# Kernel tuning notes

Measured on AMD Instinct MI355X. Metric: run time of the kernel, lower is better.

Reference implementation:

```python
import jax, jax.numpy as jnp
import numpy as np
from jax import lax

K = 3            # RFAConv kernel size
CIN = 66         # RFAConv in_channel = c2/2 + 2
UP = 64          # up channel count = c2/2
BN_EPS = 1e-5


def conv2d(x, w, stride=1, padding=0, groups=1, bias=None):
    out = lax.conv_general_dilated(
        x, w, (stride, stride), [(padding, padding), (padding, padding)],
        dimension_numbers=("NCHW", "OIHW", "NCHW"), feature_group_count=groups)
    if bias is not None:
        out = out + bias[None, :, None, None]
    return out


def avgpool3(x):
    # AvgPool2d(kernel=3, pad=1, stride=1), count_include_pad=True -> /9 everywhere
    s = lax.reduce_window(x, 0.0, lax.add, (1, 1, 3, 3), (1, 1, 1, 1),
                          [(0, 0), (0, 0), (1, 1), (1, 1)])
    return s / 9.0


def setup_inputs() -> dict:
    key = jax.random.key(0)
    ks = jax.random.split(key, 8)
    c1, c2 = 64, 128
    inp = {
        "x": jax.random.normal(ks[0], (8, c1, 256, 256), jnp.float32),
        "w_squeeze": jax.random.normal(ks[1], (c2, 4 * c1, 1, 1), jnp.float32) * 0.05,
        "w_gw": jax.random.normal(ks[2], (CIN * K * K, 1, 1, 1), jnp.float32) * 0.3,
        "w_gf": jax.random.normal(ks[3], (CIN * K * K, 1, K, K), jnp.float32) * 0.3,
        "bn_gamma": jnp.ones((CIN * K * K,), jnp.float32),
        "bn_beta": jnp.zeros((CIN * K * K,), jnp.float32),
        "bn_mean": jnp.zeros((CIN * K * K,), jnp.float32),
        "bn_var": jnp.ones((CIN * K * K,), jnp.float32),
        "w_conv": jax.random.normal(ks[4], (UP, CIN, K, K), jnp.float32) * 0.05,
        "b_conv": jnp.zeros((UP,), jnp.float32),
    }
    return inp


def reference(x, w_squeeze, w_gw, w_gf, bn_gamma, bn_beta, bn_mean, bn_var,
              w_conv, b_conv):
    # space_to_depth: [B,C,H,W] -> [B,4C,H/2,W/2]
    x = jnp.concatenate([x[..., ::2, ::2], x[..., 1::2, ::2],
                         x[..., ::2, 1::2], x[..., 1::2, 1::2]], axis=1)
    # squeeze0: 1x1 conv 4*c1 -> c2
    x = conv2d(x, w_squeeze)
    up, low = x[:, :UP], x[:, UP:]

    # AddCoords (with_r=False): append normalized xx (width) and yy (height)
    b, _, h, w = up.shape
    xx = (jnp.arange(w, dtype=up.dtype) / (w - 1) * 2.0 - 1.0)
    yy = (jnp.arange(h, dtype=up.dtype) / (h - 1) * 2.0 - 1.0)
    xx = jnp.broadcast_to(xx[None, None, None, :], (b, 1, h, w))
    yy = jnp.broadcast_to(yy[None, None, :, None], (b, 1, h, w))
    up = jnp.concatenate([up, xx, yy], axis=1)   # [b, 66, h, w]

    # RFAConv
    weight = conv2d(avgpool3(up), w_gw, groups=CIN)          # [b, 594, h, w]
    weight = jax.nn.softmax(weight.reshape(b, CIN, K * K, h, w), axis=2)

    feat = conv2d(up, w_gf, stride=1, padding=1, groups=CIN)  # [b, 594, h, w]
    scale = bn_gamma / jnp.sqrt(bn_var + BN_EPS)
    shift = bn_beta - bn_mean * scale
    feat = jax.nn.relu(feat * scale[None, :, None, None] + shift[None, :, None, None])
    feat = feat.reshape(b, CIN, K * K, h, w)

    wd = feat * weight
    # rearrange 'b c (n1 n2) h w -> b c (h n1) (w n2)'
    wd = wd.reshape(b, CIN, K, K, h, w).transpose(0, 1, 4, 2, 5, 3)
    wd = wd.reshape(b, CIN, h * K, w * K)
    up = conv2d(wd, w_conv, stride=K, bias=b_conv)            # [b, 64, h, w]

    y = jnp.concatenate([up, low], axis=1)                    # [b, 128, h, w]
    # channel shuffle: gather even channels then odd channels
    bb, n, hh, ww = y.shape
    y = y.reshape(bb, n // 2, 2, hh, ww)
    return jnp.concatenate([y[:, :, 0], y[:, :, 1]], axis=1)
```

## Files before the change

### kernel.cpp

```cpp
#include <hip/hip_runtime.h>
#include <math.h>

typedef __attribute__((ext_vector_type(8))) short short8;
typedef __attribute__((ext_vector_type(4))) float f32x4;

#define B 8
#define H 128
#define W 128
#define UPC 64
#define CIN 66
#define BN_EPS 1e-5f

#define BSQ_U16  ((size_t)16777216)
#define BSQ_CNT  32768
#define BF_U16   (BSQ_U16 + BSQ_CNT)
#define BF_CNT   38912
#define SC_F     ((size_t)8424448)
#define SH_F     (SC_F + 594)

static __device__ __forceinline__ unsigned short f2bf(float f) {
    unsigned u = __float_as_uint(f);
    u += 0x7fffu + ((u >> 16) & 1u);
    return (unsigned short)(u >> 16);
}
static __device__ __forceinline__ unsigned pack2(float lo, float hi) {
    return __builtin_amdgcn_perm(__float_as_uint(hi) + 0x8000u,
                                 __float_as_uint(lo) + 0x8000u, 0x07060302u);
}

__global__ void prep_kernel(const float* __restrict__ w_squeeze,
                            const float* __restrict__ gamma,
                            const float* __restrict__ beta,
                            const float* __restrict__ mean,
                            const float* __restrict__ var,
                            const float* __restrict__ w_conv,
                            float* __restrict__ ws)
{
    unsigned short* wsu = (unsigned short*)ws;
    int tid = blockIdx.x * blockDim.x + threadIdx.x;
    int nth = gridDim.x * blockDim.x;

    for (int idx = tid; idx < BSQ_CNT; idx += nth) {
        int j = idx & 7, lane = (idx >> 3) & 63, r = idx >> 9;
        int nt = r & 7, kc = r >> 3;
        int k = kc * 32 + ((lane >> 4) << 3) + j;
        int n = nt * 16 + (lane & 15);
        wsu[BSQ_U16 + idx] = f2bf(w_squeeze[n * 256 + k]);
    }
    for (int idx = tid; idx < BF_CNT; idx += nth) {
        int j = idx & 7, lane = (idx >> 3) & 63, r = idx >> 9;
        int nt = r & 3, ks = r >> 2;
        int k = ks * 32 + ((lane >> 4) << 3) + j;
        int n = nt * 16 + (lane & 15);
        float v = (k < 594) ? w_conv[n * 594 + k] : 0.f;
        wsu[BF_U16 + idx] = f2bf(v);
    }
    for (int i = tid; i < CIN * 9; i += nth) {
        float sc = gamma[i] / sqrtf(var[i] + BN_EPS);
        ws[SC_F + i] = sc;
        ws[SH_F + i] = beta[i] - mean[i] * sc;
    }
}

__global__ __launch_bounds__(256, 4) void squeeze_mfma(
    const float* __restrict__ x,
    float* __restrict__ wsp,
    float* __restrict__ out)
{
    __shared__ uint4 As[32 * 64];

    const int m0 = blockIdx.x * 64;
    const int w0 = m0 & 127;
    const int h  = (m0 >> 7) & 127;
    const int b  = m0 >> 14;
    const int tid  = threadIdx.x;
    const int lane = tid & 63;
    const int wv   = tid >> 6;
    const int oct = tid >> 5;
    const int pp  = tid & 31;

    float4 v[2][8];
#pragma unroll
    for (int gy = 0; gy < 2; ++gy)
#pragma unroll
        for (int i = 0; i < 8; ++i)
            v[gy][i] = *(const float4*)(x +
                (size_t)(b * 64 + oct * 8 + i) * 65536 +
                (2 * h + gy) * 256 + 2 * w0 + 4 * pp);

#pragma unroll
    for (int gy = 0; gy < 2; ++gy)
#pragma unroll
        for (int gx = 0; gx < 2; ++gx)
#pragma unroll
            for (int p = 0; p < 2; ++p) {
                const int comp = p * 2 + gx;
                uint4 u;
                u.x = pack2(((const float*)&v[gy][0])[comp], ((const float*)&v[gy][1])[comp]);
                u.y = pack2(((const float*)&v[gy][2])[comp], ((const float*)&v[gy][3])[comp]);
                u.z = pack2(((const float*)&v[gy][4])[comp], ((const float*)&v[gy][5])[comp]);
                u.w = pack2(((const float*)&v[gy][6])[comp], ((const float*)&v[gy][7])[comp]);
                As[((gy + 2 * gx) * 8 + oct) * 64 + 2 * pp + p] = u;
            }

    const unsigned short* bsq = (const unsigned short*)wsp + BSQ_U16;
    short8 breg[2][8];
#pragma unroll
    for (int ks = 0; ks < 8; ++ks)
#pragma unroll
        for (int j = 0; j < 2; ++j)
            breg[j][ks] = *(const short8*)(bsq +
                (size_t)((ks * 8 + (2 * wv + j)) * 64 + lane) * 8);

    __syncthreads();

    const int q = lane >> 4, m = lane & 15;
    f32x4 acc[4][2];
#pragma unroll
    for (int mt = 0; mt < 4; ++mt)
#pragma unroll
        for (int j = 0; j < 2; ++j) acc[mt][j] = (f32x4){0.f, 0.f, 0.f, 0.f};

#pragma unroll
    for (int ks = 0; ks < 8; ++ks)
#pragma unroll
        for (int mt = 0; mt < 4; ++mt) {
            short8 a = *(const short8*)&As[(ks * 4 + q) * 64 + mt * 16 + m];
            acc[mt][0] = __builtin_amdgcn_mfma_f32_16x16x32_bf16(a, breg[0][ks], acc[mt][0], 0, 0, 0);
            acc[mt][1] = __builtin_amdgcn_mfma_f32_16x16x32_bf16(a, breg[1][ks], acc[mt][1], 0, 0, 0);
        }

    if (wv < 2) {
        unsigned short* upw = (unsigned short*)wsp;
#pragma unroll
        for (int j = 0; j < 2; ++j) {
            const int oc = (2 * wv + j) * 16 + m;
#pragma unroll
            for (int mt = 0; mt < 4; ++mt) {
                uint2 st;
                st.x = pack2(acc[mt][j][0], acc[mt][j][1]);
                st.y = pack2(acc[mt][j][2], acc[mt][j][3]);
                *(uint2*)(upw + (size_t)(b * 64 + oc) * 16384 + h * 128
                          + (w0 + mt * 16 + q * 4)) = st;
            }
        }
    } else {
#pragma unroll
        for (int j = 0; j < 2; ++j) {
            const int oc = (2 * wv + j) * 16 + m;
            const int lc = oc - 64;
            const int ch = (lc & 1) ? (96 + ((lc - 1) >> 1)) : (32 + (lc >> 1));
#pragma unroll
            for (int mt = 0; mt < 4; ++mt) {
                float4 st = {acc[mt][j][0], acc[mt][j][1], acc[mt][j][2], acc[mt][j][3]};
                *(float4*)(out + ((size_t)(b * 128 + ch) * 128 + h) * 128
                           + (w0 + mt * 16 + q * 4)) = st;
            }
        }
    }
}

__device__ __forceinline__ void fs_from_n(
    int cu, const float n[9],
    const float* __restrict__ w_gw, const float* __restrict__ w_gf,
    const float* __restrict__ scp, const float* __restrict__ shp,
    float fs[9])
{
    const float p = (n[0] + n[1] + n[2] + n[3] + n[4] + n[5] + n[6] + n[7] + n[8]) * (1.f / 9.f);
    const float* gw = w_gw + cu * 9;
    const float* gf = w_gf + cu * 81;
    const float* sc = scp + cu * 9;
    const float* sh = shp + cu * 9;
    float e[9], se = 0.f;
#pragma unroll
    for (int j = 0; j < 9; ++j) { e[j] = __expf(p * gw[j]); se += e[j]; }
    const float sinv = 1.f / se;
#pragma unroll
    for (int j = 0; j < 9; ++j) {
        float cv = n[0] * gf[j * 9 + 0];
        cv = fmaf(n[1], gf[j * 9 + 1], cv); cv = fmaf(n[2], gf[j * 9 + 2], cv);
        cv = fmaf(n[3], gf[j * 9 + 3], cv); cv = fmaf(n[4], gf[j * 9 + 4], cv);
        cv = fmaf(n[5], gf[j * 9 + 5], cv); cv = fmaf(n[6], gf[j * 9 + 6], cv);
        cv = fmaf(n[7], gf[j * 9 + 7], cv); cv = fmaf(n[8], gf[j * 9 + 8], cv);
        float f = fmaf(cv, sc[j], sh[j]);
        fs[j] = fmaxf(f, 0.f) * (e[j] * sinv);
    }
}

__device__ __forceinline__ void pack_into(unsigned* pk, int ci, const float fs[9], float& carry)
{
    const int off = 9 * ci;
    if ((ci & 1) == 0) {
#pragma unroll
        for (int t = 0; t < 4; ++t) pk[off / 2 + t] = pack2(fs[2 * t], fs[2 * t + 1]);
        carry = fs[8];
    } else {
        pk[(off - 1) / 2] = pack2(carry, fs[0]);
#pragma unroll
        for (int t = 0; t < 4; ++t) pk[(off + 1) / 2 + t] = pack2(fs[1 + 2 * t], fs[2 + 2 * t]);
    }
}

template<bool BORDER>
__device__ __forceinline__ void chunk_fs(
    int cs, int wv, int lane, int h0, int w0,
    const unsigned short* __restrict__ upb,
    const float* __restrict__ w_gw, const float* __restrict__ w_gf,
    const float* __restrict__ scp, const float* __restrict__ shp,
    unsigned pk[36])
{
    const int px = lane & 7, py = lane >> 3;
    const int gy0 = h0 + py - 1;
    const int gxc = w0 + px;
    float carry = 0.f;

    if (!BORDER) {
        const int gx0 = (gxc - 1) & ~1;
        const unsigned sh = (gxc & 1) ? 0u : 16u;
        const size_t rowoff = (size_t)gy0 * 128 + gx0;
#pragma unroll
        for (int ci = 0; ci < 8; ++ci) {
            const int cu = __builtin_amdgcn_readfirstlane(cs + 8 * wv + ci);
            const unsigned short* cb = upb + (size_t)cu * 16384 + rowoff;
            float n[9];
#pragma unroll
            for (int dy = 0; dy < 3; ++dy) {
                const uint2 v = *(const uint2*)(cb + dy * 128);
                unsigned long long t = (((unsigned long long)v.y) << 32) | v.x;
                t >>= sh;
                n[dy * 3 + 0] = __uint_as_float((unsigned)t << 16);
                n[dy * 3 + 1] = __uint_as_float((unsigned)t & 0xffff0000u);
                n[dy * 3 + 2] = __uint_as_float((unsigned)(t >> 32) << 16);
            }
            float fs[9];
            fs_from_n(cu, n, w_gw, w_gf, scp, shp, fs);
            pack_into(pk, ci, fs, carry);
        }
    } else {
#pragma unroll
        for (int ci = 0; ci < 8; ++ci) {
            const int cu = __builtin_amdgcn_readfirstlane(cs + 8 * wv + ci);
            const unsigned short* cb = upb + (size_t)cu * 16384;
            float n[9];
#pragma unroll
            for (int dy = 0; dy < 3; ++dy)
#pragma unroll
                for (int dx = 0; dx < 3; ++dx) {
                    const int gy = gy0 + dy, gx = gxc - 1 + dx;
                    const bool ok = ((unsigned)gy < 128u) & ((unsigned)gx < 128u);
                    const int cy = min(max(gy, 0), 127), cx = min(max(gx, 0), 127);
                    const float f = __uint_as_float((unsigned)cb[cy * 128 + cx] << 16);
                    n[dy * 3 + dx] = ok ? f : 0.f;
                }
            float fs[9];
            fs_from_n(cu, n, w_gw, w_gf, scp, shp, fs);
            pack_into(pk, ci, fs, carry);
        }
    }
}

__device__ __forceinline__ void coord_n(int which, int h0, int w0, int lane, float n[9])
{
    const int px = lane & 7, py = lane >> 3;
#pragma unroll
    for (int dy = 0; dy < 3; ++dy)
#pragma unroll
        for (int dx = 0; dx < 3; ++dx) {
            const int gy = h0 + py - 1 + dy, gx = w0 + px - 1 + dx;
            const bool ok = ((unsigned)gy < 128u) & ((unsigned)gx < 128u);
            const float v = (which == 0) ? (gx * (2.f / 127.f) - 1.f)
                                         : (gy * (2.f / 127.f) - 1.f);
            n[dy * 3 + dx] = ok ? v : 0.f;
        }
}

template<int NSTEPS>
__device__ __forceinline__ void do_mfma(
    int base, const uint4* As, const unsigned short* __restrict__ bfw,
    int wv, int lane, f32x4 acc[2][2])
{
    const int q = lane >> 4, m = lane & 15;
    const int ntb = (wv >> 1) * 2;
    const int pt0 = (wv & 1) * 2;
#pragma unroll
    for (int ks = 0; ks < NSTEPS; ++ks) {
        short8 b0 = *(const short8*)(bfw + (size_t)(((base + ks) * 4 + ntb + 0) * 64 + lane) * 8);
        short8 b1 = *(const short8*)(bfw + (size_t)(((base + ks) * 4 + ntb + 1) * 64 + lane) * 8);
#pragma unroll
        for (int mt = 0; mt < 2; ++mt) {
            short8 a = *(const short8*)&As[(ks * 4 + q) * 64 + (pt0 + mt) * 16 + m];
            acc[mt][0] = __builtin_amdgcn_mfma_f32_16x16x32_bf16(a, b0, acc[mt][0], 0, 0, 0);
            acc[mt][1] = __builtin_amdgcn_mfma_f32_16x16x32_bf16(a, b1, acc[mt][1], 0, 0, 0);
        }
    }
}

__global__ __launch_bounds__(256, 4) void fused_mfma(
    const float* __restrict__ wsp,
    const float* __restrict__ w_gw,
    const float* __restrict__ w_gf,
    const float* __restrict__ b_conv,
    float* __restrict__ out)
{
    __shared__ uint4 As[40 * 64];

    const int bx = blockIdx.x;
    const int w0 = (bx & 15) * 8;
    const int h0 = ((bx >> 4) & 15) * 8;
    const int b  = bx >> 8;
    const int tid = threadIdx.x, lane = tid & 63, wv = tid >> 6;
    const bool interior = (h0 > 0) & (h0 < 120) & (w0 > 0) & (w0 < 120);

    const unsigned short* upb = (const unsigned short*)wsp + (size_t)b * UPC * 16384;
    const float* scp = wsp + SC_F;
    const float* shp = wsp + SH_F;
    const unsigned short* bfw = (const unsigned short*)wsp + BF_U16;

    f32x4 acc[2][2];
#pragma unroll
    for (int mt = 0; mt < 2; ++mt)
#pragma unroll
        for (int j = 0; j < 2; ++j) acc[mt][j] = (f32x4){0.f, 0.f, 0.f, 0.f};

    {
        unsigned pk[36];
        if (interior) chunk_fs<false>(0, wv, lane, h0, w0, upb, w_gw, w_gf, scp, shp, pk);
        else          chunk_fs<true >(0, wv, lane, h0, w0, upb, w_gw, w_gf, scp, shp, pk);
        __syncthreads();
#pragma unroll
        for (int kb = 0; kb < 9; ++kb)
            As[(9 * wv + kb) * 64 + lane] =
                (uint4){pk[4 * kb], pk[4 * kb + 1], pk[4 * kb + 2], pk[4 * kb + 3]};
        __syncthreads();
        do_mfma<9>(0, As, bfw, wv, lane, acc);
    }

    {
        unsigned pk[36];
        if (interior) chunk_fs<false>(32, wv, lane, h0, w0, upb, w_gw, w_gf, scp, shp, pk);
        else          chunk_fs<true >(32, wv, lane, h0, w0, upb, w_gw, w_gf, scp, shp, pk);

        float fsA[9], fsB[9];
        if (wv == 3) {
            float n2[9];
            coord_n(0, h0, w0, lane, n2);
            fs_from_n(64, n2, w_gw, w_gf, scp, shp, fsA);
            coord_n(1, h0, w0, lane, n2);
            fs_from_n(65, n2, w_gw, w_gf, scp, shp, fsB);
        }
        __syncthreads();
#pragma unroll
        for (int kb = 0; kb < 9; ++kb)
            As[(9 * wv + kb) * 64 + lane] =
                (uint4){pk[4 * kb], pk[4 * kb + 1], pk[4 * kb + 2], pk[4 * kb + 3]};
        if (wv == 3) {
            uint4 v;
            v.x = pack2(fsA[0], fsA[1]); v.y = pack2(fsA[2], fsA[3]);
            v.z = pack2(fsA[4], fsA[5]); v.w = pack2(fsA[6], fsA[7]);
            As[36 * 64 + lane] = v;
            v.x = pack2(fsA[8], fsB[0]); v.y = pack2(fsB[1], fsB[2]);
            v.z = pack2(fsB[3], fsB[4]); v.w = pack2(fsB[5], fsB[6]);
            As[37 * 64 + lane] = v;
            v.x = pack2(fsB[7], fsB[8]); v.y = 0u; v.z = 0u; v.w = 0u;
            As[38 * 64 + lane] = v;
            v.x = 0u; v.y = 0u; v.z = 0u; v.w = 0u;
            As[39 * 64 + lane] = v;
        }
        __syncthreads();
        do_mfma<10>(9, As, bfw, wv, lane, acc);
    }

    const int q = lane >> 4, m = lane & 15;
    const int ntb = (wv >> 1) * 2, pt0 = (wv & 1) * 2;
#pragma unroll
    for (int mt = 0; mt < 2; ++mt)
#pragma unroll
        for (int j = 0; j < 2; ++j) {
            const int oc = (ntb + j) * 16 + m;
            const float bias = b_conv[oc];
            const int ch = (oc & 1) ? (64 + (oc >> 1)) : (oc >> 1);
#pragma unroll
            for (int r = 0; r < 4; ++r) {
                const int pix = (pt0 + mt) * 16 + q * 4 + r;
                out[((size_t)((b * 128 + ch) * 128 + (h0 + (pix >> 3)))) * 128
                    + (w0 + (pix & 7))] = acc[mt][j][r] + bias;
            }
        }
}

extern "C" void kernel_launch(void* const* d_in, const int* in_sizes, int n_in,
                              void* d_out, int out_size, void* d_ws, size_t ws_size,
                              hipStream_t stream)
{
    const float* x         = (const float*)d_in[0];
    const float* w_squeeze = (const float*)d_in[1];
    const float* w_gw      = (const float*)d_in[2];
    const float* w_gf      = (const float*)d_in[3];
    const float* gamma     = (const float*)d_in[4];
    const float* beta      = (const float*)d_in[5];
    const float* mean      = (const float*)d_in[6];
    const float* var       = (const float*)d_in[7];
    const float* w_conv    = (const float*)d_in[8];
    const float* b_conv    = (const float*)d_in[9];
    float* out = (float*)d_out;
    float* ws  = (float*)d_ws;

    prep_kernel<<<160, 256, 0, stream>>>(w_squeeze, gamma, beta, mean, var, w_conv, ws);
    squeeze_mfma<<<(B * H * W) / 64, 256, 0, stream>>>(x, ws, out);
    fused_mfma<<<B * 16 * 16, 256, 0, stream>>>(ws, w_gw, w_gf, b_conv, out);
}
```

Measured before the change: 329.3 us.

## Pad up planes, precompute coord-channel contribution, overlap loads with MFMA

Squeeze output is now written into zero-padded 130x132 bf16 planes, which removes the border branch in the fused kernel. The two coordinate channels' contribution to the final conv is precomputed per pixel in the prep kernel and added in the epilogue, so the fused kernel needs only 18 MFMA steps. The fused kernel now issues the second chunk's global loads before the first MFMA group to overlap them. Other changes: batch-interleaved block indexing, rolling B-register prefetch in squeeze with launch bounds raised to 5, and vectorized float4 output stores. The extra prep work and the extra read of the precomputed buffer add cost in exchange.

New measurement: 341.0 us. 1.04x slower.

```diff
diff --git a/kernel.cpp b/kernel.cpp
--- a/kernel.cpp
+++ b/kernel.cpp
@@ -4,17 +4,17 @@
 typedef __attribute__((ext_vector_type(8))) short short8;
 typedef __attribute__((ext_vector_type(4))) float f32x4;
 
-#define B 8
-#define H 128
-#define W 128
-#define UPC 64
 #define CIN 66
 #define BN_EPS 1e-5f
 
+#define PLROW 132
+#define PLN   17160
+
+#define CO_F     ((size_t)4500000)
 #define BSQ_U16  ((size_t)16777216)
 #define BSQ_CNT  32768
 #define BF_U16   (BSQ_U16 + BSQ_CNT)
-#define BF_CNT   38912
+#define BF_CNT   36864
 #define SC_F     ((size_t)8424448)
 #define SH_F     (SC_F + 594)
 
@@ -33,12 +33,14 @@
                             const float* __restrict__ beta,
                             const float* __restrict__ mean,
                             const float* __restrict__ var,
+                            const float* __restrict__ w_gw,
+                            const float* __restrict__ w_gf,
                             const float* __restrict__ w_conv,
                             float* __restrict__ ws)
 {
     unsigned short* wsu = (unsigned short*)ws;
-    int tid = blockIdx.x * blockDim.x + threadIdx.x;
-    int nth = gridDim.x * blockDim.x;
+    const int tid = blockIdx.x * blockDim.x + threadIdx.x;
+    const int nth = gridDim.x * blockDim.x;
 
     for (int idx = tid; idx < BSQ_CNT; idx += nth) {
         int j = idx & 7, lane = (idx >> 3) & 63, r = idx >> 9;
@@ -52,27 +54,83 @@
         int nt = r & 3, ks = r >> 2;
         int k = ks * 32 + ((lane >> 4) << 3) + j;
         int n = nt * 16 + (lane & 15);
-        float v = (k < 594) ? w_conv[n * 594 + k] : 0.f;
-        wsu[BF_U16 + idx] = f2bf(v);
+        wsu[BF_U16 + idx] = f2bf(w_conv[n * 594 + k]);
     }
     for (int i = tid; i < CIN * 9; i += nth) {
         float sc = gamma[i] / sqrtf(var[i] + BN_EPS);
         ws[SC_F + i] = sc;
         ws[SH_F + i] = beta[i] - mean[i] * sc;
     }
-}
-
-__global__ __launch_bounds__(256, 4) void squeeze_mfma(
+    for (int idx = tid; idx < 512 * 388; idx += nth) {
+        int plane = idx / 388, r = idx - plane * 388;
+        unsigned* pb = (unsigned*)(wsu + (size_t)plane * PLN);
+        if (r < 66)       pb[r] = 0u;
+        else if (r < 132) pb[8514 + (r - 66)] = 0u;
+        else {
+            int rr = (r - 132) >> 1, side = (r - 132) & 1;
+            pb[(rr + 1) * 66 + (side ? 65 : 0)] = 0u;
+        }
+    }
+    if (tid < 16384) {
+        const int h = tid >> 7, w = tid & 127;
+        float fsA[9], fsB[9];
+#pragma unroll
+        for (int c = 0; c < 2; ++c) {
+            const int cu = 64 + c;
+            float n[9];
+#pragma unroll
+            for (int dy = 0; dy < 3; ++dy)
+#pragma unroll
+                for (int dx = 0; dx < 3; ++dx) {
+                    const int gy = h - 1 + dy, gx = w - 1 + dx;
+                    const bool ok = ((unsigned)gy < 128u) & ((unsigned)gx < 128u);
+                    const float v = (c == 0) ? (gx * (2.f / 127.f) - 1.f)
+                                             : (gy * (2.f / 127.f) - 1.f);
+                    n[dy * 3 + dx] = ok ? v : 0.f;
+                }
+            const float p = (n[0]+n[1]+n[2]+n[3]+n[4]+n[5]+n[6]+n[7]+n[8]) * (1.f/9.f);
+            const float* gw = w_gw + cu * 9;
+            const float* gf = w_gf + cu * 81;
+            float e[9], se = 0.f;
+#pragma unroll
+            for (int j = 0; j < 9; ++j) { e[j] = __expf(p * gw[j]); se += e[j]; }
+            const float sinv = 1.f / se;
+            float* fs = c ? fsB : fsA;
+#pragma unroll
+            for (int j = 0; j < 9; ++j) {
+                float cv = 0.f;
+#pragma unroll
+                for (int i = 0; i < 9; ++i) cv = fmaf(n[i], gf[j * 9 + i], cv);
+                const float sc = gamma[cu * 9 + j] / sqrtf(var[cu * 9 + j] + BN_EPS);
+                const float sh = beta[cu * 9 + j] - mean[cu * 9 + j] * sc;
+                const float f = fmaf(cv, sc, sh);
+                fs[j] = fmaxf(f, 0.f) * (e[j] * sinv);
+            }
+        }
+#pragma unroll 1
+        for (int oc = 0; oc < 64; ++oc) {
+            const float* wc = w_conv + oc * 594;
+            float s = 0.f;
+#pragma unroll
+            for (int j = 0; j < 9; ++j)
+                s = fmaf(fsA[j], wc[576 + j], fmaf(fsB[j], wc[585 + j], s));
+            ws[CO_F + (size_t)oc * 16384 + tid] = s;
+        }
+    }
+}
+
+__global__ __launch_bounds__(256, 5) void squeeze_mfma(
     const float* __restrict__ x,
     float* __restrict__ wsp,
     float* __restrict__ out)
 {
     __shared__ uint4 As[32 * 64];
 
-    const int m0 = blockIdx.x * 64;
-    const int w0 = m0 & 127;
-    const int h  = (m0 >> 7) & 127;
-    const int b  = m0 >> 14;
+    const int bx  = blockIdx.x;
+    const int b   = bx & 7;
+    const int pos = bx >> 3;
+    const int h   = pos >> 1;
+    const int w0  = (pos & 1) * 64;
     const int tid  = threadIdx.x;
     const int lane = tid & 63;
     const int wv   = tid >> 6;
@@ -103,17 +161,9 @@
                 As[((gy + 2 * gx) * 8 + oct) * 64 + 2 * pp + p] = u;
             }
 
+    __syncthreads();
+
     const unsigned short* bsq = (const unsigned short*)wsp + BSQ_U16;
-    short8 breg[2][8];
-#pragma unroll
-    for (int ks = 0; ks < 8; ++ks)
-#pragma unroll
-        for (int j = 0; j < 2; ++j)
-            breg[j][ks] = *(const short8*)(bsq +
-                (size_t)((ks * 8 + (2 * wv + j)) * 64 + lane) * 8);
-
-    __syncthreads();
-
     const int q = lane >> 4, m = lane & 15;
     f32x4 acc[4][2];
 #pragma unroll
@@ -121,14 +171,23 @@
 #pragma unroll
         for (int j = 0; j < 2; ++j) acc[mt][j] = (f32x4){0.f, 0.f, 0.f, 0.f};
 
-#pragma unroll
-    for (int ks = 0; ks < 8; ++ks)
+    short8 b0 = *(const short8*)(bsq + (size_t)((2 * wv + 0) * 64 + lane) * 8);
+    short8 b1 = *(const short8*)(bsq + (size_t)((2 * wv + 1) * 64 + lane) * 8);
+#pragma unroll
+    for (int ks = 0; ks < 8; ++ks) {
+        short8 nb0, nb1;
+        if (ks < 7) {
+            nb0 = *(const short8*)(bsq + (size_t)(((ks + 1) * 8 + 2 * wv + 0) * 64 + lane) * 8);
+            nb1 = *(const short8*)(bsq + (size_t)(((ks + 1) * 8 + 2 * wv + 1) * 64 + lane) * 8);
+        }
 #pragma unroll
         for (int mt = 0; mt < 4; ++mt) {
             short8 a = *(const short8*)&As[(ks * 4 + q) * 64 + mt * 16 + m];
-            acc[mt][0] = __builtin_amdgcn_mfma_f32_16x16x32_bf16(a, breg[0][ks], acc[mt][0], 0, 0, 0);
-            acc[mt][1] = __builtin_amdgcn_mfma_f32_16x16x32_bf16(a, breg[1][ks], acc[mt][1], 0, 0, 0);
-        }
+            acc[mt][0] = __builtin_amdgcn_mfma_f32_16x16x32_bf16(a, b0, acc[mt][0], 0, 0, 0);
+            acc[mt][1] = __builtin_amdgcn_mfma_f32_16x16x32_bf16(a, b1, acc[mt][1], 0, 0, 0);
+        }
+        if (ks < 7) { b0 = nb0; b1 = nb1; }
+    }
 
     if (wv < 2) {
         unsigned short* upw = (unsigned short*)wsp;
@@ -140,8 +199,8 @@
                 uint2 st;
                 st.x = pack2(acc[mt][j][0], acc[mt][j][1]);
                 st.y = pack2(acc[mt][j][2], acc[mt][j][3]);
-                *(uint2*)(upw + (size_t)(b * 64 + oc) * 16384 + h * 128
-                          + (w0 + mt * 16 + q * 4)) = st;
+                *(uint2*)(upw + (size_t)(b * 64 + oc) * PLN + (size_t)(h + 1) * PLROW
+                          + (w0 + mt * 16 + q * 4 + 2)) = st;
             }
         }
     } else {
@@ -201,77 +260,47 @@
     }
 }
 
-template<bool BORDER>
-__device__ __forceinline__ void chunk_fs(
-    int cs, int wv, int lane, int h0, int w0,
-    const unsigned short* __restrict__ upb,
+__device__ __forceinline__ void chunk_loads(
+    int cbase, int lane, int h0, int w0,
+    const unsigned short* __restrict__ upb, uint2 vr[8][3])
+{
+    const int px = lane & 7, py = lane >> 3;
+    const size_t rowoff = (size_t)(h0 + py) * PLROW + (size_t)((w0 + px + 1) & ~1);
+#pragma unroll
+    for (int ci = 0; ci < 8; ++ci) {
+        const int cu = __builtin_amdgcn_readfirstlane(cbase + ci);
+        const unsigned short* cb = upb + (size_t)cu * PLN + rowoff;
+#pragma unroll
+        for (int dy = 0; dy < 3; ++dy)
+            vr[ci][dy] = *(const uint2*)(cb + dy * PLROW);
+    }
+}
+
+__device__ __forceinline__ void chunk_compute(
+    int cbase, int lane, const uint2 vr[8][3],
     const float* __restrict__ w_gw, const float* __restrict__ w_gf,
     const float* __restrict__ scp, const float* __restrict__ shp,
     unsigned pk[36])
 {
-    const int px = lane & 7, py = lane >> 3;
-    const int gy0 = h0 + py - 1;
-    const int gxc = w0 + px;
+    const unsigned sh = (lane & 1) ? 0u : 16u;
     float carry = 0.f;
-
-    if (!BORDER) {
-        const int gx0 = (gxc - 1) & ~1;
-        const unsigned sh = (gxc & 1) ? 0u : 16u;
-        const size_t rowoff = (size_t)gy0 * 128 + gx0;
-#pragma unroll
-        for (int ci = 0; ci < 8; ++ci) {
-            const int cu = __builtin_amdgcn_readfirstlane(cs + 8 * wv + ci);
-            const unsigned short* cb = upb + (size_t)cu * 16384 + rowoff;
-            float n[9];
-#pragma unroll
-            for (int dy = 0; dy < 3; ++dy) {
-                const uint2 v = *(const uint2*)(cb + dy * 128);
-                unsigned long long t = (((unsigned long long)v.y) << 32) | v.x;
-                t >>= sh;
-                n[dy * 3 + 0] = __uint_as_float((unsigned)t << 16);
-                n[dy * 3 + 1] = __uint_as_float((unsigned)t & 0xffff0000u);
-                n[dy * 3 + 2] = __uint_as_float((unsigned)(t >> 32) << 16);
-            }
-            float fs[9];
-            fs_from_n(cu, n, w_gw, w_gf, scp, shp, fs);
-            pack_into(pk, ci, fs, carry);
-        }
-    } else {
-#pragma unroll
-        for (int ci = 0; ci < 8; ++ci) {
-            const int cu = __builtin_amdgcn_readfirstlane(cs + 8 * wv + ci);
-            const unsigned short* cb = upb + (size_t)cu * 16384;
-            float n[9];
-#pragma unroll
-            for (int dy = 0; dy < 3; ++dy)
-#pragma unroll
-                for (int dx = 0; dx < 3; ++dx) {
-                    const int gy = gy0 + dy, gx = gxc - 1 + dx;
-                    const bool ok = ((unsigned)gy < 128u) & ((unsigned)gx < 128u);
-                    const int cy = min(max(gy, 0), 127), cx = min(max(gx, 0), 127);
-                    const float f = __uint_as_float((unsigned)cb[cy * 128 + cx] << 16);
-                    n[dy * 3 + dx] = ok ? f : 0.f;
-                }
-            float fs[9];
-            fs_from_n(cu, n, w_gw, w_gf, scp, shp, fs);
-            pack_into(pk, ci, fs, carry);
-        }
-    }
-}
-
-__device__ __forceinline__ void coord_n(int which, int h0, int w0, int lane, float n[9])
-{
-    const int px = lane & 7, py = lane >> 3;
-#pragma unroll
-    for (int dy = 0; dy < 3; ++dy)
-#pragma unroll
-        for (int dx = 0; dx < 3; ++dx) {
-            const int gy = h0 + py - 1 + dy, gx = w0 + px - 1 + dx;
-            const bool ok = ((unsigned)gy < 128u) & ((unsigned)gx < 128u);
-            const float v = (which == 0) ? (gx * (2.f / 127.f) - 1.f)
-                                         : (gy * (2.f / 127.f) - 1.f);
-            n[dy * 3 + dx] = ok ? v : 0.f;
-        }
+#pragma unroll
+    for (int ci = 0; ci < 8; ++ci) {
+        const int cu = __builtin_amdgcn_readfirstlane(cbase + ci);
+        float n[9];
+#pragma unroll
+        for (int dy = 0; dy < 3; ++dy) {
+            const uint2 vv = vr[ci][dy];
+            unsigned long long t = (((unsigned long long)vv.y) << 32) | vv.x;
+            t >>= sh;
+            n[dy * 3 + 0] = __uint_as_float((unsigned)t << 16);
+            n[dy * 3 + 1] = __uint_as_float((unsigned)t & 0xffff0000u);
+            n[dy * 3 + 2] = __uint_as_float((unsigned)(t >> 32) << 16);
+        }
+        float fs[9];
+        fs_from_n(cu, n, w_gw, w_gf, scp, shp, fs);
+        pack_into(pk, ci, fs, carry);
+    }
 }
 
 template<int NSTEPS>
@@ -302,16 +331,16 @@
     const float* __restrict__ b_conv,
     float* __restrict__ out)
 {
-    __shared__ uint4 As[40 * 64];
+    __shared__ uint4 As[36 * 64];
 
     const int bx = blockIdx.x;
-    const int w0 = (bx & 15) * 8;
-    const int h0 = ((bx >> 4) & 15) * 8;
-    const int b  = bx >> 8;
+    const int b  = bx & 7;
+    const int t  = bx >> 3;
+    const int w0 = (t & 15) * 8;
+    const int h0 = ((t >> 4) & 15) * 8;
     const int tid = threadIdx.x, lane = tid & 63, wv = tid >> 6;
-    const bool interior = (h0 > 0) & (h0 < 120) & (w0 > 0) & (w0 < 120);
-
-    const unsigned short* upb = (const unsigned short*)wsp + (size_t)b * UPC * 16384;
+
+    const unsigned short* upb = (const unsigned short*)wsp + (size_t)b * 64 * PLN;
     const float* scp = wsp + SC_F;
     const float* shp = wsp + SH_F;
     const unsigned short* bfw = (const unsigned short*)wsp + BF_U16;
@@ -322,69 +351,47 @@
 #pragma unroll
         for (int j = 0; j < 2; ++j) acc[mt][j] = (f32x4){0.f, 0.f, 0.f, 0.f};
 
-    {
-        unsigned pk[36];
-        if (interior) chunk_fs<false>(0, wv, lane, h0, w0, upb, w_gw, w_gf, scp, shp, pk);
-        else          chunk_fs<true >(0, wv, lane, h0, w0, upb, w_gw, w_gf, scp, shp, pk);
-        __syncthreads();
-#pragma unroll
-        for (int kb = 0; kb < 9; ++kb)
-            As[(9 * wv + kb) * 64 + lane] =
-                (uint4){pk[4 * kb], pk[4 * kb + 1], pk[4 * kb + 2], pk[4 * kb + 3]};
-        __syncthreads();
-        do_mfma<9>(0, As, bfw, wv, lane, acc);
-    }
-
-    {
-        unsigned pk[36];
-        if (interior) chunk_fs<false>(32, wv, lane, h0, w0, upb, w_gw, w_gf, scp, shp, pk);
-        else          chunk_fs<true >(32, wv, lane, h0, w0, upb, w_gw, w_gf, scp, shp, pk);
-
-        float fsA[9], fsB[9];
-        if (wv == 3) {
-            float n2[9];
-            coord_n(0, h0, w0, lane, n2);
-            fs_from_n(64, n2, w_gw, w_gf, scp, shp, fsA);
-            coord_n(1, h0, w0, lane, n2);
-            fs_from_n(65, n2, w_gw, w_gf, scp, shp, fsB);
-        }
-        __syncthreads();
-#pragma unroll
-        for (int kb = 0; kb < 9; ++kb)
-            As[(9 * wv + kb) * 64 + lane] =
-                (uint4){pk[4 * kb], pk[4 * kb + 1], pk[4 * kb + 2], pk[4 * kb + 3]};
-        if (wv == 3) {
-            uint4 v;
-            v.x = pack2(fsA[0], fsA[1]); v.y = pack2(fsA[2], fsA[3]);
-            v.z = pack2(fsA[4], fsA[5]); v.w = pack2(fsA[6], fsA[7]);
-            As[36 * 64 + lane] = v;
-            v.x = pack2(fsA[8], fsB[0]); v.y = pack2(fsB[1], fsB[2]);
-            v.z = pack2(fsB[3], fsB[4]); v.w = pack2(fsB[5], fsB[6]);
-            As[37 * 64 + lane] = v;
-            v.x = pack2(fsB[7], fsB[8]); v.y = 0u; v.z = 0u; v.w = 0u;
-            As[38 * 64 + lane] = v;
-            v.x = 0u; v.y = 0u; v.z = 0u; v.w = 0u;
-            As[39 * 64 + lane] = v;
-        }
-        __syncthreads();
-        do_mfma<10>(9, As, bfw, wv, lane, acc);
-    }
+    uint2 vr[8][3];
+    unsigned pk[36];
+
+    chunk_loads(8 * wv, lane, h0, w0, upb, vr);
+    chunk_compute(8 * wv, lane, vr, w_gw, w_gf, scp, shp, pk);
+#pragma unroll
+    for (int kb = 0; kb < 9; ++kb)
+        As[(9 * wv + kb) * 64 + lane] =
+            (uint4){pk[4 * kb], pk[4 * kb + 1], pk[4 * kb + 2], pk[4 * kb + 3]};
+    __syncthreads();
+
+    chunk_loads(32 + 8 * wv, lane, h0, w0, upb, vr);
+    do_mfma<9>(0, As, bfw, wv, lane, acc);
+    chunk_compute(32 + 8 * wv, lane, vr, w_gw, w_gf, scp, shp, pk);
+    __syncthreads();
+#pragma unroll
+    for (int kb = 0; kb < 9; ++kb)
+        As[(9 * wv + kb) * 64 + lane] =
+            (uint4){pk[4 * kb], pk[4 * kb + 1], pk[4 * kb + 2], pk[4 * kb + 3]};
+    __syncthreads();
+    do_mfma<9>(9, As, bfw, wv, lane, acc);
 
     const int q = lane >> 4, m = lane & 15;
     const int ntb = (wv >> 1) * 2, pt0 = (wv & 1) * 2;
+    const float* co = wsp + CO_F;
 #pragma unroll
     for (int mt = 0; mt < 2; ++mt)
 #pragma unroll
         for (int j = 0; j < 2; ++j) {
             const int oc = (ntb + j) * 16 + m;
+            const int ch = (oc & 1) ? (64 + (oc >> 1)) : (oc >> 1);
+            const int row = h0 + (pt0 + mt) * 2 + (q >> 1);
+            const int col = w0 + (q & 1) * 4;
+            const size_t pix = (size_t)row * 128 + col;
+            const float4 cv = *(const float4*)(co + (size_t)oc * 16384 + pix);
             const float bias = b_conv[oc];
-            const int ch = (oc & 1) ? (64 + (oc >> 1)) : (oc >> 1);
-#pragma unroll
-            for (int r = 0; r < 4; ++r) {
-                const int pix = (pt0 + mt) * 16 + q * 4 + r;
-                out[((size_t)((b * 128 + ch) * 128 + (h0 + (pix >> 3)))) * 128
-                    + (w0 + (pix & 7))] = acc[mt][j][r] + bias;
-            }
+            float4 st = { acc[mt][j][0] + bias + cv.x,
+                          acc[mt][j][1] + bias + cv.y,
+                          acc[mt][j][2] + bias + cv.z,
+                          acc[mt][j][3] + bias + cv.w };
+            *(float4*)(out + (size_t)(b * 128 + ch) * 16384 + pix) = st;
         }
 }
 
@@ -405,7 +412,8 @@
     float* out = (float*)d_out;
     float* ws  = (float*)d_ws;
 
-    prep_kernel<<<160, 256, 0, stream>>>(w_squeeze, gamma, beta, mean, var, w_conv, ws);
-    squeeze_mfma<<<(B * H * W) / 64, 256, 0, stream>>>(x, ws, out);
-    fused_mfma<<<B * 16 * 16, 256, 0, stream>>>(ws, w_gw, w_gf, b_conv, out);
-}
+    prep_kernel<<<160, 256, 0, stream>>>(w_squeeze, gamma, beta, mean, var,
+                                         w_gw, w_gf, w_conv, ws);
+    squeeze_mfma<<<2048, 256, 0, stream>>>(x, ws, out);
+    fused_mfma<<<2048, 256, 0, stream>>>(ws, w_gw, w_gf, b_conv, out);
+}
```
